# Optimization experiments

Hardware: AMD Instinct MI355X
Metric: run time of the kernel (lower is better)

Reference implementation:

```python
import jax, jax.numpy as jnp
import numpy as np

N = 16384
N_ITER = 10
TAU = 1e-3  # LM initial damping factor


def _skew(w):
    z = jnp.zeros((), w.dtype)
    return jnp.stack([
        jnp.stack([z, -w[2], w[1]]),
        jnp.stack([w[2], z, -w[0]]),
        jnp.stack([-w[1], w[0], z]),
    ])


def se3_exp(x):
    # x = [omega (3), v (3)] -> 4x4 SE3 (lie_se3_to_SE3)
    w, v = x[:3], x[3:]
    th2 = jnp.dot(w, w)
    th = jnp.sqrt(th2)
    small = th < 1e-8
    ths = jnp.where(small, jnp.ones_like(th), th)
    A = jnp.where(small, 1.0 - th2 / 6.0, jnp.sin(ths) / ths)
    B = jnp.where(small, 0.5 - th2 / 24.0, (1.0 - jnp.cos(ths)) / ths ** 2)
    C = jnp.where(small, 1.0 / 6.0 - th2 / 120.0, (ths - jnp.sin(ths)) / ths ** 3)
    W = _skew(w)
    W2 = W @ W
    I = jnp.eye(3, dtype=x.dtype)
    R = I + A * W + B * W2
    V = I + B * W + C * W2
    t = V @ v
    T = jnp.eye(4, dtype=x.dtype).at[:3, :3].set(R).at[:3, 3].set(t)
    return T


def _res_jac(x, ref_pts, trg_pts, trg_normals):
    T = se3_exp(x)
    R, t = T[:3, :3], T[:3, 3]
    # dist_association: ref cloud transformed by inv(T_est), nearest target point
    Ri, ti = R.T, -R.T @ t
    ref_t = ref_pts @ Ri.T + ti  # [N,3]
    d2 = ((ref_t ** 2).sum(-1)[:, None]
          + (trg_pts ** 2).sum(-1)[None, :]
          - 2.0 * (ref_t @ trg_pts.T))  # [N_ref, N_trg] -- dominant memory traffic
    trg_ids = jnp.argmin(d2, axis=1)  # src_ids == arange(N_ref)
    # residual: dot(n_trg_transformed, ref - trg_transformed) at correspondences
    trg_t = trg_pts @ R.T + t
    n_t = trg_normals @ R.T
    n = n_t[trg_ids]          # [N,3] gather
    p = trg_t[trg_ids]        # [N,3] gather
    r = jnp.sum(n * (ref_pts - p), axis=1)  # [N]
    # J = n^T @ j_3d(ref_pts)  ==  [cross(p_ref, n), n]  (closed form of 1x3x6 matmuls)
    J = jnp.concatenate([jnp.cross(ref_pts, n), n], axis=1)  # [N,6]
    return r, J


def reference(ref_pts, trg_pts, trg_normals):
    dtype = ref_pts.dtype
    x = jnp.zeros(6, dtype=dtype)
    r, J = _res_jac(x, ref_pts, trg_pts, trg_normals)
    F = jnp.sum(r ** 2)
    H0 = J.T @ J
    mu = TAU * jnp.max(jnp.diag(H0))
    nu = jnp.asarray(2.0, dtype)
    I6 = jnp.eye(6, dtype=dtype)
    for _ in range(N_ITER):
        H = J.T @ J
        g = J.T @ r
        dx = jnp.linalg.solve(H + mu * I6, -g)
        x_new = x + dx
        r_new, J_new = _res_jac(x_new, ref_pts, trg_pts, trg_normals)
        F_new = jnp.sum(r_new ** 2)
        denom = jnp.dot(dx, mu * dx - g)
        rho = (F - F_new) / jnp.where(jnp.abs(denom) < 1e-12, 1e-12, denom)
        accept = rho > 0.0
        x = jnp.where(accept, x_new, x)
        r = jnp.where(accept, r_new, r)
        J = jnp.where(accept, J_new, J)
        F = jnp.where(accept, F_new, F)
        mu = jnp.where(accept,
                       mu * jnp.maximum(1.0 / 3.0, 1.0 - (2.0 * rho - 1.0) ** 3),
                       mu * nu)
        nu = jnp.where(accept, jnp.asarray(2.0, dtype), 2.0 * nu)
    T = se3_exp(x)
    cost = jnp.mean(r ** 2)  # cost_fun(residual_fun(x,...))
    return T, cost


def setup_inputs() -> dict:
    key = jax.random.key(0)
    k1, k2 = jax.random.split(key)
    ref_pts = jax.random.normal(k1, (N, 3), dtype=jnp.float32)
    # target = slightly rotated/translated copy so ICP has a meaningful solution
    ang = 0.05
    R_true = np.array([[np.cos(ang), -np.sin(ang), 0.0],
                       [np.sin(ang), np.cos(ang), 0.0],
                       [0.0, 0.0, 1.0]], dtype=np.float32)
    t_true = np.array([0.02, -0.01, 0.03], dtype=np.float32)
    trg_pts = ref_pts @ jnp.asarray(R_true).T + jnp.asarray(t_true)
    n = jax.random.normal(k2, (N, 3), dtype=jnp.float32)
    trg_normals = n / jnp.linalg.norm(n, axis=1, keepdims=True)
    return {"ref_pts": ref_pts, "trg_pts": trg_pts, "trg_normals": trg_normals}
```

## Files before the change

### kernel.cpp

```cpp
#include <hip/hip_runtime.h>
#include <stdint.h>

#define N_PTS 16384
#define TAU_C 0.001f
#define N_ITER 10
#define BJ 512
#define MI 4
#define NGROUP (BJ / 8)

struct State {
  float x[6];
  float xc[6];
  float dx[6];
  float Rc[9];
  float tc[3];
  float H[21];
  float g[6];
  float F, mu, nu;
};

__device__ void se3_exp_rt(const float* x, float* R, float* t) {
  float wx = x[0], wy = x[1], wz = x[2];
  float vx = x[3], vy = x[4], vz = x[5];
  float th2 = wx*wx + wy*wy + wz*wz;
  float th = sqrtf(th2);
  float A, B, C;
  if (th < 1e-8f) {
    A = 1.0f - th2 / 6.0f;
    B = 0.5f - th2 / 24.0f;
    C = 1.0f / 6.0f - th2 / 120.0f;
  } else {
    float s = sinf(th), c = cosf(th);
    A = s / th;
    B = (1.0f - c) / th2;
    C = (th - s) / (th2 * th);
  }
  float W[9]  = {0.f, -wz, wy,  wz, 0.f, -wx,  -wy, wx, 0.f};
  float W2[9];
  #pragma unroll
  for (int r = 0; r < 3; r++)
    #pragma unroll
    for (int c = 0; c < 3; c++)
      W2[3*r+c] = W[3*r+0]*W[0+c] + W[3*r+1]*W[3+c] + W[3*r+2]*W[6+c];
  float V[9];
  #pragma unroll
  for (int k = 0; k < 9; k++) {
    float I = (k == 0 || k == 4 || k == 8) ? 1.f : 0.f;
    R[k] = I + A * W[k] + B * W2[k];
    V[k] = I + B * W[k] + C * W2[k];
  }
  t[0] = V[0]*vx + V[1]*vy + V[2]*vz;
  t[1] = V[3]*vx + V[4]*vy + V[5]*vz;
  t[2] = V[6]*vx + V[7]*vy + V[8]*vz;
}

__global__ void prep_kernel(const float* __restrict__ trg,
                            float4* __restrict__ packed,
                            unsigned long long* __restrict__ keys,
                            State* st) {
  int i = blockIdx.x * blockDim.x + threadIdx.x;
  if (i < N_PTS) {
    float tx = trg[3*i], ty = trg[3*i+1], tz = trg[3*i+2];
    packed[i] = make_float4(-2.f*tx, -2.f*ty, -2.f*tz, tx*tx + ty*ty + tz*tz);
    keys[i] = 0xFFFFFFFFFFFFFFFFULL;
  }
  if (blockIdx.x == 0 && threadIdx.x == 0) {
    #pragma unroll
    for (int k = 0; k < 6; k++) { st->x[k] = 0.f; st->xc[k] = 0.f; st->dx[k] = 0.f; }
    #pragma unroll
    for (int k = 0; k < 9; k++) st->Rc[k] = (k % 4 == 0) ? 1.f : 0.f;
    st->tc[0] = st->tc[1] = st->tc[2] = 0.f;
    st->nu = 2.f;
  }
}

__global__ __launch_bounds__(256) void nn_kernel(const float* __restrict__ ref,
                                                 const float4* __restrict__ packed,
                                                 const State* __restrict__ st,
                                                 unsigned long long* __restrict__ keys) {
  __shared__ float4 tile[BJ];
  const int tid = threadIdx.x;
  const int jbase = blockIdx.y * BJ;
  #pragma unroll
  for (int k = 0; k < BJ/256; k++)
    tile[tid + 256*k] = packed[jbase + tid + 256*k];

  const float R00 = st->Rc[0], R01 = st->Rc[1], R02 = st->Rc[2];
  const float R10 = st->Rc[3], R11 = st->Rc[4], R12 = st->Rc[5];
  const float R20 = st->Rc[6], R21 = st->Rc[7], R22 = st->Rc[8];
  const float t0 = st->tc[0], t1 = st->tc[1], t2 = st->tc[2];

  const int i0 = blockIdx.x * (256 * MI) + tid;
  float px[MI], py[MI], pz[MI];
  #pragma unroll
  for (int m = 0; m < MI; m++) {
    int i = i0 + 256*m;
    float ax = ref[3*i] - t0, ay = ref[3*i+1] - t1, az = ref[3*i+2] - t2;
    px[m] = R00*ax + R10*ay + R20*az;
    py[m] = R01*ax + R11*ay + R21*az;
    pz[m] = R02*ax + R12*ay + R22*az;
  }
  __syncthreads();

  float best[MI];
  int bg[MI];
  #pragma unroll
  for (int m = 0; m < MI; m++) { best[m] = 3.4e38f; bg[m] = 0; }

  #pragma unroll 2
  for (int g = 0; g < NGROUP; g++) {
    float4 tq[8];
    #pragma unroll
    for (int k = 0; k < 8; k++) tq[k] = tile[8*g + k];
    #pragma unroll
    for (int m = 0; m < MI; m++) {
      float s[8];
      #pragma unroll
      for (int k = 0; k < 8; k++) {
        float v = fmaf(px[m], tq[k].x, tq[k].w);
        v = fmaf(py[m], tq[k].y, v);
        s[k] = fmaf(pz[m], tq[k].z, v);
      }
      float a = fminf(fminf(s[0], s[1]), s[2]);
      float b = fminf(fminf(s[3], s[4]), s[5]);
      float c = fminf(fminf(s[6], s[7]), a);
      float gm = fminf(b, c);
      if (gm < best[m]) { best[m] = gm; bg[m] = g; }
    }
  }

  #pragma unroll
  for (int m = 0; m < MI; m++) {
    int jb = 8 * bg[m];
    int bj = 0;
    #pragma unroll
    for (int k = 7; k >= 0; k--) {
      float4 tq = tile[jb + k];
      float v = fmaf(px[m], tq.x, tq.w);
      v = fmaf(py[m], tq.y, v);
      v = fmaf(pz[m], tq.z, v);
      if (v == best[m]) bj = k;
    }
    int i = i0 + 256*m;
    unsigned ub = __float_as_uint(best[m]);
    ub = (ub & 0x80000000u) ? ~ub : (ub | 0x80000000u);
    unsigned long long key = ((unsigned long long)ub << 32) |
                             (unsigned long long)(unsigned)(jbase + jb + bj);
    atomicMin(&keys[i], key);
  }
}

__global__ __launch_bounds__(256) void accum_part_kernel(const float* __restrict__ ref,
                                                         const float* __restrict__ trg,
                                                         const float* __restrict__ nrm,
                                                         unsigned long long* __restrict__ keys,
                                                         const State* __restrict__ st,
                                                         float* __restrict__ partials) {
  const int tid = threadIdx.x;
  const int i = blockIdx.x * 256 + tid;

  const float R00 = st->Rc[0], R01 = st->Rc[1], R02 = st->Rc[2];
  const float R10 = st->Rc[3], R11 = st->Rc[4], R12 = st->Rc[5];
  const float R20 = st->Rc[6], R21 = st->Rc[7], R22 = st->Rc[8];
  const float t0 = st->tc[0], t1 = st->tc[1], t2 = st->tc[2];

  unsigned long long key = keys[i];
  keys[i] = 0xFFFFFFFFFFFFFFFFULL;
  int j = (int)(unsigned)(key & 0xFFFFFFFFULL);

  float nx0 = nrm[3*j], ny0 = nrm[3*j+1], nz0 = nrm[3*j+2];
  float qx = trg[3*j], qy = trg[3*j+1], qz = trg[3*j+2];
  float nx = R00*nx0 + R01*ny0 + R02*nz0;
  float ny = R10*nx0 + R11*ny0 + R12*nz0;
  float nz = R20*nx0 + R21*ny0 + R22*nz0;
  float pxx = R00*qx + R01*qy + R02*qz + t0;
  float pyy = R10*qx + R11*qy + R12*qz + t1;
  float pzz = R20*qx + R21*qy + R22*qz + t2;

  float rx = ref[3*i], ry = ref[3*i+1], rz = ref[3*i+2];
  float dxx = rx - pxx, dyy = ry - pyy, dzz = rz - pzz;
  float r = nx*dxx + ny*dyy + nz*dzz;

  float J[6];
  J[0] = ry*nz - rz*ny;
  J[1] = rz*nx - rx*nz;
  J[2] = rx*ny - ry*nx;
  J[3] = nx; J[4] = ny; J[5] = nz;

  float acc[28];
  int c21 = 0;
  #pragma unroll
  for (int a = 0; a < 6; a++)
    #pragma unroll
    for (int b = a; b < 6; b++)
      acc[c21++] = J[a] * J[b];
  #pragma unroll
  for (int a = 0; a < 6; a++) acc[21+a] = J[a] * r;
  acc[27] = r * r;

  #pragma unroll
  for (int kk = 0; kk < 28; kk++) {
    float v = acc[kk];
    for (int off = 32; off; off >>= 1) v += __shfl_down(v, off);
    acc[kk] = v;
  }
  __shared__ float red[4][28];
  int wave = tid >> 6, lane = tid & 63;
  if (lane == 0) {
    #pragma unroll
    for (int kk = 0; kk < 28; kk++) red[wave][kk] = acc[kk];
  }
  __syncthreads();
  if (tid < 28) {
    partials[tid * 64 + blockIdx.x] =
        red[0][tid] + red[1][tid] + red[2][tid] + red[3][tid];
  }
}

__global__ __launch_bounds__(64) void lm_kernel(const float* __restrict__ partials,
                                                State* st, float* out, int mode) {
  __shared__ float tot[28];
  const int tid = threadIdx.x;
  if (tid < 28) {
    float s = 0.f;
    #pragma unroll
    for (int b = 0; b < 64; b++) s += partials[tid * 64 + b];
    tot[tid] = s;
  }
  __syncthreads();

  if (tid == 0) {
    float Fn = tot[27];
    float mu, nu;

    if (mode == 0) {
      #pragma unroll
      for (int k = 0; k < 6; k++) st->x[k] = st->xc[k];
      #pragma unroll
      for (int k = 0; k < 21; k++) st->H[k] = tot[k];
      #pragma unroll
      for (int k = 0; k < 6; k++) st->g[k] = tot[21+k];
      st->F = Fn;
      float md = tot[0];
      md = fmaxf(md, tot[6]); md = fmaxf(md, tot[11]); md = fmaxf(md, tot[15]);
      md = fmaxf(md, tot[18]); md = fmaxf(md, tot[20]);
      mu = TAU_C * md;
      nu = 2.f;
    } else {
      mu = st->mu; nu = st->nu;
      float denom = 0.f;
      #pragma unroll
      for (int k = 0; k < 6; k++) denom += st->dx[k] * (mu * st->dx[k] - st->g[k]);
      if (fabsf(denom) < 1e-12f) denom = 1e-12f;
      float rho = (st->F - Fn) / denom;
      if (rho > 0.f) {
        #pragma unroll
        for (int k = 0; k < 6; k++) st->x[k] = st->xc[k];
        #pragma unroll
        for (int k = 0; k < 21; k++) st->H[k] = tot[k];
        #pragma unroll
        for (int k = 0; k < 6; k++) st->g[k] = tot[21+k];
        st->F = Fn;
        float tcube = 2.f * rho - 1.f;
        mu = mu * fmaxf(1.f / 3.f, 1.f - tcube * tcube * tcube);
        nu = 2.f;
      } else {
        mu = mu * nu;
        nu = 2.f * nu;
      }
    }
    st->mu = mu; st->nu = nu;

    if (mode < N_ITER) {
      float A[6][7];
      int c21 = 0;
      #pragma unroll
      for (int a = 0; a < 6; a++)
        #pragma unroll
        for (int b = a; b < 6; b++) { A[a][b] = st->H[c21]; A[b][a] = st->H[c21]; c21++; }
      #pragma unroll
      for (int a = 0; a < 6; a++) { A[a][a] += mu; A[a][6] = -st->g[a]; }
      #pragma unroll
      for (int col = 0; col < 6; col++) {
        float inv = 1.f / A[col][col];
        #pragma unroll
        for (int rI = 0; rI < 6; rI++) {
          if (rI > col) {
            float f = A[rI][col] * inv;
            #pragma unroll
            for (int cc = 0; cc < 7; cc++)
              if (cc >= col) A[rI][cc] -= f * A[col][cc];
          }
        }
      }
      float d[6];
      #pragma unroll
      for (int rI = 5; rI >= 0; rI--) {
        float s = A[rI][6];
        #pragma unroll
        for (int cc = 0; cc < 6; cc++)
          if (cc > rI) s -= A[rI][cc] * d[cc];
        d[rI] = s / A[rI][rI];
      }
      float Rn[9], tn[3];
      #pragma unroll
      for (int k = 0; k < 6; k++) { st->dx[k] = d[k]; st->xc[k] = st->x[k] + d[k]; }
      se3_exp_rt(st->xc, Rn, tn);
      #pragma unroll
      for (int k = 0; k < 9; k++) st->Rc[k] = Rn[k];
      #pragma unroll
      for (int k = 0; k < 3; k++) st->tc[k] = tn[k];
    } else {
      float Rn[9], tn[3];
      se3_exp_rt(st->x, Rn, tn);
      out[0] = Rn[0]; out[1] = Rn[1]; out[2]  = Rn[2]; out[3]  = tn[0];
      out[4] = Rn[3]; out[5] = Rn[4]; out[6]  = Rn[5]; out[7]  = tn[1];
      out[8] = Rn[6]; out[9] = Rn[7]; out[10] = Rn[8]; out[11] = tn[2];
      out[12] = 0.f; out[13] = 0.f; out[14] = 0.f; out[15] = 1.f;
      out[16] = st->F / (float)N_PTS;
    }
  }
}

extern "C" void kernel_launch(void* const* d_in, const int* in_sizes, int n_in,
                              void* d_out, int out_size, void* d_ws, size_t ws_size,
                              hipStream_t stream) {
  const float* ref = (const float*)d_in[0];
  const float* trg = (const float*)d_in[1];
  const float* nrm = (const float*)d_in[2];
  float* out = (float*)d_out;

  char* ws = (char*)d_ws;
  float4* packed = (float4*)ws;
  unsigned long long* keys = (unsigned long long*)(ws + 262144);
  float* partials = (float*)(ws + 262144 + 131072);
  State* st = (State*)(ws + 262144 + 131072 + 8192);

  prep_kernel<<<64, 256, 0, stream>>>(trg, packed, keys, st);
  for (int e = 0; e <= N_ITER; e++) {
    nn_kernel<<<dim3(N_PTS / (256 * MI), N_PTS / BJ), 256, 0, stream>>>(ref, packed, st, keys);
    accum_part_kernel<<<64, 256, 0, stream>>>(ref, trg, nrm, keys, st, partials);
    lm_kernel<<<1, 64, 0, stream>>>(partials, st, out, e);
  }
}
```

Before: 370.9 us.

## Use packed FP32 FMA with SoA tile layout and fuse LM solve into accumulation

```diff
diff --git a/kernel.cpp b/kernel.cpp
--- a/kernel.cpp
+++ b/kernel.cpp
@@ -7,6 +7,17 @@
 #define BJ 512
 #define MI 4
 #define NGROUP (BJ / 8)
+#define NACC 64
+
+typedef float f2 __attribute__((ext_vector_type(2)));
+
+union F4 { float4 q; f2 h[2]; };
+
+__device__ inline f2 pk_fma(f2 a, f2 b, f2 c) {
+  f2 d;
+  asm("v_pk_fma_f32 %0, %1, %2, %3" : "=v"(d) : "v"(a), "v"(b), "v"(c));
+  return d;
+}
 
 struct State {
   float x[6];
@@ -55,13 +66,18 @@
 }
 
 __global__ void prep_kernel(const float* __restrict__ trg,
-                            float4* __restrict__ packed,
+                            float* __restrict__ packed,
                             unsigned long long* __restrict__ keys,
+                            unsigned* __restrict__ counter,
                             State* st) {
   int i = blockIdx.x * blockDim.x + threadIdx.x;
   if (i < N_PTS) {
     float tx = trg[3*i], ty = trg[3*i+1], tz = trg[3*i+2];
-    packed[i] = make_float4(-2.f*tx, -2.f*ty, -2.f*tz, tx*tx + ty*ty + tz*tz);
+    int g = i >> 3, k = i & 7, base = g * 32;
+    packed[base + k]      = -2.f * tx;
+    packed[base + 8 + k]  = -2.f * ty;
+    packed[base + 16 + k] = -2.f * tz;
+    packed[base + 24 + k] = tx*tx + ty*ty + tz*tz;
     keys[i] = 0xFFFFFFFFFFFFFFFFULL;
   }
   if (blockIdx.x == 0 && threadIdx.x == 0) {
@@ -71,19 +87,23 @@
     for (int k = 0; k < 9; k++) st->Rc[k] = (k % 4 == 0) ? 1.f : 0.f;
     st->tc[0] = st->tc[1] = st->tc[2] = 0.f;
     st->nu = 2.f;
+    *counter = 0u;
   }
 }
 
 __global__ __launch_bounds__(256) void nn_kernel(const float* __restrict__ ref,
-                                                 const float4* __restrict__ packed,
+                                                 const float* __restrict__ packed,
                                                  const State* __restrict__ st,
                                                  unsigned long long* __restrict__ keys) {
-  __shared__ float4 tile[BJ];
+  __shared__ float tileF[BJ * 4];
   const int tid = threadIdx.x;
   const int jbase = blockIdx.y * BJ;
-  #pragma unroll
-  for (int k = 0; k < BJ/256; k++)
-    tile[tid + 256*k] = packed[jbase + tid + 256*k];
+  {
+    float4* t4 = (float4*)tileF;
+    const float4* src = (const float4*)(packed + (size_t)jbase * 4);
+    t4[tid]       = src[tid];
+    t4[tid + 256] = src[tid + 256];
+  }
 
   const float R00 = st->Rc[0], R01 = st->Rc[1], R02 = st->Rc[2];
   const float R10 = st->Rc[3], R11 = st->Rc[4], R12 = st->Rc[5];
@@ -91,14 +111,17 @@
   const float t0 = st->tc[0], t1 = st->tc[1], t2 = st->tc[2];
 
   const int i0 = blockIdx.x * (256 * MI) + tid;
-  float px[MI], py[MI], pz[MI];
+  f2 px2[MI], py2[MI], pz2[MI];
   #pragma unroll
   for (int m = 0; m < MI; m++) {
     int i = i0 + 256*m;
     float ax = ref[3*i] - t0, ay = ref[3*i+1] - t1, az = ref[3*i+2] - t2;
-    px[m] = R00*ax + R10*ay + R20*az;
-    py[m] = R01*ax + R11*ay + R21*az;
-    pz[m] = R02*ax + R12*ay + R22*az;
+    float px = R00*ax + R10*ay + R20*az;
+    float py = R01*ax + R11*ay + R21*az;
+    float pz = R02*ax + R12*ay + R22*az;
+    px2[m] = (f2){px, px};
+    py2[m] = (f2){py, py};
+    pz2[m] = (f2){pz, pz};
   }
   __syncthreads();
 
@@ -109,53 +132,61 @@
 
   #pragma unroll 2
   for (int g = 0; g < NGROUP; g++) {
-    float4 tq[8];
-    #pragma unroll
-    for (int k = 0; k < 8; k++) tq[k] = tile[8*g + k];
+    const float4* gp = (const float4*)&tileF[g * 32];
+    F4 X0, X1, Y0, Y1, Z0, Z1, W0, W1;
+    X0.q = gp[0]; X1.q = gp[1];
+    Y0.q = gp[2]; Y1.q = gp[3];
+    Z0.q = gp[4]; Z1.q = gp[5];
+    W0.q = gp[6]; W1.q = gp[7];
     #pragma unroll
     for (int m = 0; m < MI; m++) {
-      float s[8];
-      #pragma unroll
-      for (int k = 0; k < 8; k++) {
-        float v = fmaf(px[m], tq[k].x, tq[k].w);
-        v = fmaf(py[m], tq[k].y, v);
-        s[k] = fmaf(pz[m], tq[k].z, v);
-      }
-      float a = fminf(fminf(s[0], s[1]), s[2]);
-      float b = fminf(fminf(s[3], s[4]), s[5]);
-      float c = fminf(fminf(s[6], s[7]), a);
-      float gm = fminf(b, c);
+      f2 s0 = pk_fma(pz2[m], Z0.h[0], pk_fma(py2[m], Y0.h[0], pk_fma(px2[m], X0.h[0], W0.h[0])));
+      f2 s1 = pk_fma(pz2[m], Z0.h[1], pk_fma(py2[m], Y0.h[1], pk_fma(px2[m], X0.h[1], W0.h[1])));
+      f2 s2 = pk_fma(pz2[m], Z1.h[0], pk_fma(py2[m], Y1.h[0], pk_fma(px2[m], X1.h[0], W1.h[0])));
+      f2 s3 = pk_fma(pz2[m], Z1.h[1], pk_fma(py2[m], Y1.h[1], pk_fma(px2[m], X1.h[1], W1.h[1])));
+      float a = fminf(s0.x, s0.y);
+      float b = fminf(s1.x, s1.y);
+      float c = fminf(s2.x, s2.y);
+      float d = fminf(s3.x, s3.y);
+      float gm = fminf(fminf(a, b), fminf(c, d));
       if (gm < best[m]) { best[m] = gm; bg[m] = g; }
     }
   }
 
   #pragma unroll
   for (int m = 0; m < MI; m++) {
-    int jb = 8 * bg[m];
+    const float4* gp = (const float4*)&tileF[bg[m] * 32];
+    F4 X0, X1, Y0, Y1, Z0, Z1, W0, W1;
+    X0.q = gp[0]; X1.q = gp[1];
+    Y0.q = gp[2]; Y1.q = gp[3];
+    Z0.q = gp[4]; Z1.q = gp[5];
+    W0.q = gp[6]; W1.q = gp[7];
+    f2 s0 = pk_fma(pz2[m], Z0.h[0], pk_fma(py2[m], Y0.h[0], pk_fma(px2[m], X0.h[0], W0.h[0])));
+    f2 s1 = pk_fma(pz2[m], Z0.h[1], pk_fma(py2[m], Y0.h[1], pk_fma(px2[m], X0.h[1], W0.h[1])));
+    f2 s2 = pk_fma(pz2[m], Z1.h[0], pk_fma(py2[m], Y1.h[0], pk_fma(px2[m], X1.h[0], W1.h[0])));
+    f2 s3 = pk_fma(pz2[m], Z1.h[1], pk_fma(py2[m], Y1.h[1], pk_fma(px2[m], X1.h[1], W1.h[1])));
+    float sv[8] = {s0.x, s0.y, s1.x, s1.y, s2.x, s2.y, s3.x, s3.y};
     int bj = 0;
     #pragma unroll
-    for (int k = 7; k >= 0; k--) {
-      float4 tq = tile[jb + k];
-      float v = fmaf(px[m], tq.x, tq.w);
-      v = fmaf(py[m], tq.y, v);
-      v = fmaf(pz[m], tq.z, v);
-      if (v == best[m]) bj = k;
-    }
+    for (int k = 7; k >= 0; k--)
+      if (sv[k] == best[m]) bj = k;
     int i = i0 + 256*m;
     unsigned ub = __float_as_uint(best[m]);
     ub = (ub & 0x80000000u) ? ~ub : (ub | 0x80000000u);
     unsigned long long key = ((unsigned long long)ub << 32) |
-                             (unsigned long long)(unsigned)(jbase + jb + bj);
+                             (unsigned long long)(unsigned)(jbase + 8*bg[m] + bj);
     atomicMin(&keys[i], key);
   }
 }
 
-__global__ __launch_bounds__(256) void accum_part_kernel(const float* __restrict__ ref,
-                                                         const float* __restrict__ trg,
-                                                         const float* __restrict__ nrm,
-                                                         unsigned long long* __restrict__ keys,
-                                                         const State* __restrict__ st,
-                                                         float* __restrict__ partials) {
+__global__ __launch_bounds__(256) void accum_lm_kernel(const float* __restrict__ ref,
+                                                       const float* __restrict__ trg,
+                                                       const float* __restrict__ nrm,
+                                                       unsigned long long* __restrict__ keys,
+                                                       State* st,
+                                                       float* __restrict__ partials,
+                                                       unsigned* __restrict__ counter,
+                                                       float* out, int mode) {
   const int tid = threadIdx.x;
   const int i = blockIdx.x * 256 + tid;
 
@@ -211,25 +242,32 @@
     for (int kk = 0; kk < 28; kk++) red[wave][kk] = acc[kk];
   }
   __syncthreads();
-  if (tid < 28) {
-    partials[tid * 64 + blockIdx.x] =
+  if (tid < 28)
+    partials[tid * NACC + blockIdx.x] =
         red[0][tid] + red[1][tid] + red[2][tid] + red[3][tid];
-  }
-}
-
-__global__ __launch_bounds__(64) void lm_kernel(const float* __restrict__ partials,
-                                                State* st, float* out, int mode) {
+
+  __shared__ bool last;
+  __syncthreads();
+  if (tid == 0) {
+    __threadfence();
+    unsigned old = atomicAdd(counter, 1u);
+    last = (old == NACC - 1);
+  }
+  __syncthreads();
+  if (!last) return;
+
+  __threadfence();
   __shared__ float tot[28];
-  const int tid = threadIdx.x;
   if (tid < 28) {
     float s = 0.f;
     #pragma unroll
-    for (int b = 0; b < 64; b++) s += partials[tid * 64 + b];
+    for (int b = 0; b < NACC; b++) s += partials[tid * NACC + b];
     tot[tid] = s;
   }
   __syncthreads();
 
   if (tid == 0) {
+    atomicExch(counter, 0u);
     float Fn = tot[27];
     float mu, nu;
 
@@ -273,11 +311,11 @@
 
     if (mode < N_ITER) {
       float A[6][7];
-      int c21 = 0;
+      int c21b = 0;
       #pragma unroll
       for (int a = 0; a < 6; a++)
         #pragma unroll
-        for (int b = a; b < 6; b++) { A[a][b] = st->H[c21]; A[b][a] = st->H[c21]; c21++; }
+        for (int b = a; b < 6; b++) { A[a][b] = st->H[c21b]; A[b][a] = st->H[c21b]; c21b++; }
       #pragma unroll
       for (int a = 0; a < 6; a++) { A[a][a] += mu; A[a][6] = -st->g[a]; }
       #pragma unroll
@@ -331,15 +369,15 @@
   float* out = (float*)d_out;
 
   char* ws = (char*)d_ws;
-  float4* packed = (float4*)ws;
+  float* packed = (float*)ws;
   unsigned long long* keys = (unsigned long long*)(ws + 262144);
   float* partials = (float*)(ws + 262144 + 131072);
-  State* st = (State*)(ws + 262144 + 131072 + 8192);
-
-  prep_kernel<<<64, 256, 0, stream>>>(trg, packed, keys, st);
+  unsigned* counter = (unsigned*)(ws + 262144 + 131072 + 8192);
+  State* st = (State*)(ws + 262144 + 131072 + 8192 + 256);
+
+  prep_kernel<<<64, 256, 0, stream>>>(trg, packed, keys, counter, st);
   for (int e = 0; e <= N_ITER; e++) {
     nn_kernel<<<dim3(N_PTS / (256 * MI), N_PTS / BJ), 256, 0, stream>>>(ref, packed, st, keys);
-    accum_part_kernel<<<64, 256, 0, stream>>>(ref, trg, nrm, keys, st, partials);
-    lm_kernel<<<1, 64, 0, stream>>>(partials, st, out, e);
-  }
-}
+    accum_lm_kernel<<<NACC, 256, 0, stream>>>(ref, trg, nrm, keys, st, partials, counter, out, e);
+  }
+}
```

Result: slower. 456.2 us (+23.0%).

## Fuse LM solve into accumulation kernel via last-block counter, halve NN tile

Applied to the files above, without the earlier changes.

```diff
diff --git a/kernel.cpp b/kernel.cpp
--- a/kernel.cpp
+++ b/kernel.cpp
@@ -4,9 +4,10 @@
 #define N_PTS 16384
 #define TAU_C 0.001f
 #define N_ITER 10
-#define BJ 512
+#define BJ 256
 #define MI 4
 #define NGROUP (BJ / 8)
+#define NACC 64
 
 struct State {
   float x[6];
@@ -57,6 +58,7 @@
 __global__ void prep_kernel(const float* __restrict__ trg,
                             float4* __restrict__ packed,
                             unsigned long long* __restrict__ keys,
+                            unsigned* __restrict__ counter,
                             State* st) {
   int i = blockIdx.x * blockDim.x + threadIdx.x;
   if (i < N_PTS) {
@@ -71,6 +73,7 @@
     for (int k = 0; k < 9; k++) st->Rc[k] = (k % 4 == 0) ? 1.f : 0.f;
     st->tc[0] = st->tc[1] = st->tc[2] = 0.f;
     st->nu = 2.f;
+    *counter = 0u;
   }
 }
 
@@ -81,9 +84,7 @@
   __shared__ float4 tile[BJ];
   const int tid = threadIdx.x;
   const int jbase = blockIdx.y * BJ;
-  #pragma unroll
-  for (int k = 0; k < BJ/256; k++)
-    tile[tid + 256*k] = packed[jbase + tid + 256*k];
+  tile[tid] = packed[jbase + tid];
 
   const float R00 = st->Rc[0], R01 = st->Rc[1], R02 = st->Rc[2];
   const float R10 = st->Rc[3], R11 = st->Rc[4], R12 = st->Rc[5];
@@ -123,19 +124,19 @@
       }
       float a = fminf(fminf(s[0], s[1]), s[2]);
       float b = fminf(fminf(s[3], s[4]), s[5]);
-      float c = fminf(fminf(s[6], s[7]), a);
-      float gm = fminf(b, c);
+      float c = fminf(a, b);
+      float gm = fminf(fminf(s[6], s[7]), c);
       if (gm < best[m]) { best[m] = gm; bg[m] = g; }
     }
   }
 
   #pragma unroll
   for (int m = 0; m < MI; m++) {
-    int jb = 8 * bg[m];
+    const float4* gp = packed + jbase + 8 * bg[m];
     int bj = 0;
     #pragma unroll
     for (int k = 7; k >= 0; k--) {
-      float4 tq = tile[jb + k];
+      float4 tq = gp[k];
       float v = fmaf(px[m], tq.x, tq.w);
       v = fmaf(py[m], tq.y, v);
       v = fmaf(pz[m], tq.z, v);
@@ -145,17 +146,19 @@
     unsigned ub = __float_as_uint(best[m]);
     ub = (ub & 0x80000000u) ? ~ub : (ub | 0x80000000u);
     unsigned long long key = ((unsigned long long)ub << 32) |
-                             (unsigned long long)(unsigned)(jbase + jb + bj);
+                             (unsigned long long)(unsigned)(jbase + 8*bg[m] + bj);
     atomicMin(&keys[i], key);
   }
 }
 
-__global__ __launch_bounds__(256) void accum_part_kernel(const float* __restrict__ ref,
-                                                         const float* __restrict__ trg,
-                                                         const float* __restrict__ nrm,
-                                                         unsigned long long* __restrict__ keys,
-                                                         const State* __restrict__ st,
-                                                         float* __restrict__ partials) {
+__global__ __launch_bounds__(256) void accum_lm_kernel(const float* __restrict__ ref,
+                                                       const float* __restrict__ trg,
+                                                       const float* __restrict__ nrm,
+                                                       unsigned long long* __restrict__ keys,
+                                                       State* st,
+                                                       float* __restrict__ partials,
+                                                       unsigned* __restrict__ counter,
+                                                       float* out, int mode) {
   const int tid = threadIdx.x;
   const int i = blockIdx.x * 256 + tid;
 
@@ -211,25 +214,32 @@
     for (int kk = 0; kk < 28; kk++) red[wave][kk] = acc[kk];
   }
   __syncthreads();
-  if (tid < 28) {
-    partials[tid * 64 + blockIdx.x] =
+  if (tid < 28)
+    partials[tid * NACC + blockIdx.x] =
         red[0][tid] + red[1][tid] + red[2][tid] + red[3][tid];
-  }
-}
-
-__global__ __launch_bounds__(64) void lm_kernel(const float* __restrict__ partials,
-                                                State* st, float* out, int mode) {
+
+  __shared__ bool last;
+  __syncthreads();
+  if (tid == 0) {
+    __threadfence();
+    unsigned old = atomicAdd(counter, 1u);
+    last = (old == NACC - 1);
+  }
+  __syncthreads();
+  if (!last) return;
+
+  __threadfence();
   __shared__ float tot[28];
-  const int tid = threadIdx.x;
   if (tid < 28) {
     float s = 0.f;
     #pragma unroll
-    for (int b = 0; b < 64; b++) s += partials[tid * 64 + b];
+    for (int b = 0; b < NACC; b++) s += partials[tid * NACC + b];
     tot[tid] = s;
   }
   __syncthreads();
 
   if (tid == 0) {
+    atomicExch(counter, 0u);
     float Fn = tot[27];
     float mu, nu;
 
@@ -273,11 +283,11 @@
 
     if (mode < N_ITER) {
       float A[6][7];
-      int c21 = 0;
+      int c21b = 0;
       #pragma unroll
       for (int a = 0; a < 6; a++)
         #pragma unroll
-        for (int b = a; b < 6; b++) { A[a][b] = st->H[c21]; A[b][a] = st->H[c21]; c21++; }
+        for (int b = a; b < 6; b++) { A[a][b] = st->H[c21b]; A[b][a] = st->H[c21b]; c21b++; }
       #pragma unroll
       for (int a = 0; a < 6; a++) { A[a][a] += mu; A[a][6] = -st->g[a]; }
       #pragma unroll
@@ -334,12 +344,12 @@
   float4* packed = (float4*)ws;
   unsigned long long* keys = (unsigned long long*)(ws + 262144);
   float* partials = (float*)(ws + 262144 + 131072);
-  State* st = (State*)(ws + 262144 + 131072 + 8192);
-
-  prep_kernel<<<64, 256, 0, stream>>>(trg, packed, keys, st);
+  unsigned* counter = (unsigned*)(ws + 262144 + 131072 + 8192);
+  State* st = (State*)(ws + 262144 + 131072 + 8192 + 256);
+
+  prep_kernel<<<64, 256, 0, stream>>>(trg, packed, keys, counter, st);
   for (int e = 0; e <= N_ITER; e++) {
     nn_kernel<<<dim3(N_PTS / (256 * MI), N_PTS / BJ), 256, 0, stream>>>(ref, packed, st, keys);
-    accum_part_kernel<<<64, 256, 0, stream>>>(ref, trg, nrm, keys, st, partials);
-    lm_kernel<<<1, 64, 0, stream>>>(partials, st, out, e);
-  }
-}
+    accum_lm_kernel<<<NACC, 256, 0, stream>>>(ref, trg, nrm, keys, st, partials, counter, out, e);
+  }
+}
```

Result: slower. 429.5 us (+15.8%).
